# Kernel tuning notes

Measured on AMD Instinct MI355X. Metric: run time of the kernel, lower is better.

Reference implementation:

```python
import jax, jax.numpy as jnp
import numpy as np

NUM_CLASSES = 1000
EMB_DIM = 768
BATCH = 16384
EPS = 1e-8  # torch F.cosine_similarity eps


def setup_inputs() -> dict:
    key = jax.random.key(0)
    k1, k2, k3, k4 = jax.random.split(key, 4)
    embeddings = jax.random.normal(k1, (BATCH, EMB_DIM), dtype=jnp.float32)
    logits = jax.random.normal(k2, (BATCH, NUM_CLASSES), dtype=jnp.float32)
    targets = jax.random.randint(k3, (BATCH,), 0, NUM_CLASSES, dtype=jnp.int64 if jax.config.jax_enable_x64 else jnp.int32)
    centroids = jax.random.normal(k4, (NUM_CLASSES, EMB_DIM), dtype=jnp.float32)
    u = jnp.ones((1,), dtype=jnp.float32)
    return {"embeddings": embeddings, "logits": logits, "targets": targets,
            "centroids": centroids, "u": u}


def _cosine_sim(embeddings, centroids):
    # torch cosine_similarity: x / max(||x||, eps); formulated as normalize + GEMM
    en = embeddings / jnp.maximum(jnp.linalg.norm(embeddings, axis=1, keepdims=True), EPS)
    cn = centroids / jnp.maximum(jnp.linalg.norm(centroids, axis=1, keepdims=True), EPS)
    return jnp.einsum('nd,cd->nc', en, cn)  # [N, C]


def reference(embeddings, logits, targets, centroids, u):
    n_classes = centroids.shape[0]
    # cross entropy (mean reduction)
    logp = jax.nn.log_softmax(logits, axis=1)
    ce_loss = -jnp.mean(jnp.take_along_axis(logp, targets[:, None], axis=1))

    sim = _cosine_sim(embeddings, centroids)            # [N, C]
    soft_labels = jax.nn.softmax(sim, axis=1)           # [N, C]

    hard_one_hot = jax.nn.one_hot(targets, n_classes, dtype=jnp.float32)
    similarity_to_target = jnp.sum(soft_labels * hard_one_hot, axis=1)  # [N]
    discount = 1.0 - similarity_to_target
    reg_term = jnp.mean(discount) * u                   # shape (1,)

    # mse_loss(hard_one_hot, soft_labels.detach()) -- soft_labels detached
    dist_reg = jnp.mean((hard_one_hot - jax.lax.stop_gradient(soft_labels)) ** 2)

    return ce_loss + dist_reg + reg_term                # shape (1,)
```

## Files before the change

kernel.cpp:

```cpp
#include <hip/hip_runtime.h>
#include <hip/hip_bf16.h>
#include <stdint.h>

#define BATCH 16384
#define NCLS 1000
#define NPAD 1024
#define EMB 768
#define KT 12
#define BM 128
#define BN 256
#define ABYTES 8192
#define BUFB 24576
#define GEMM_BLKS 512
#define PREP_MAIN 2048
#define PREP_CENT 128

typedef __attribute__((ext_vector_type(4))) float f32x4;
typedef long v2i64 __attribute__((ext_vector_type(2)));

#define GLOAD16(g, l) __builtin_amdgcn_global_load_lds(              \
    (const __attribute__((address_space(1))) unsigned int*)(g),       \
    (__attribute__((address_space(3))) unsigned int*)(l), 16, 0, 0)

__device__ __forceinline__ float d4(float4 v) {
    return v.x*v.x + v.y*v.y + v.z*v.z + v.w*v.w;
}
__device__ __forceinline__ float e4(float4 v) {
    return __expf(v.x) + __expf(v.y) + __expf(v.z) + __expf(v.w);
}
__device__ __forceinline__ unsigned int pk8(float4 v, float s) {
    int p = 0;
    p = __builtin_amdgcn_cvt_pk_fp8_f32(v.x * s, v.y * s, p, false);
    p = __builtin_amdgcn_cvt_pk_fp8_f32(v.z * s, v.w * s, p, true);
    return (unsigned int)p;
}

__global__ __launch_bounds__(256, 4) void prep_ce(
    const float* __restrict__ emb, const float* __restrict__ cent,
    const float* __restrict__ logits, const int* __restrict__ targets,
    unsigned int* __restrict__ en8, unsigned int* __restrict__ cn8,
    float* __restrict__ ce_row)
{
    const int b    = blockIdx.x;
    const int lane = threadIdx.x & 63;
    const int w    = threadIdx.x >> 6;

    if (b < PREP_MAIN) {
        const int e0 = b * 8 + w * 2;
        const float4* a0 = (const float4*)(emb + (size_t)e0 * EMB);
        const float4* a1 = (const float4*)(emb + (size_t)(e0 + 1) * EMB);
        const float4* r0 = (const float4*)(logits + (size_t)e0 * NCLS);
        const float4* r1 = (const float4*)(logits + (size_t)(e0 + 1) * NCLS);

        float4 ea0 = a0[lane], ea1 = a0[lane + 64], ea2 = a0[lane + 128];
        float4 eb0 = a1[lane], eb1 = a1[lane + 64], eb2 = a1[lane + 128];
        float4 la0 = r0[lane], la1 = r0[lane + 64], la2 = r0[lane + 128];
        float4 lb0 = r1[lane], lb1 = r1[lane + 64], lb2 = r1[lane + 128];
        const bool has = lane < 58;
        float4 la3 = has ? r0[lane + 192] : la0;
        float4 lb3 = has ? r1[lane + 192] : lb0;
        const int t0 = targets[e0], t1 = targets[e0 + 1];
        const float xt0 = logits[(size_t)e0 * NCLS + t0];
        const float xt1 = logits[(size_t)(e0 + 1) * NCLS + t1];

        float ss0 = d4(ea0) + d4(ea1) + d4(ea2);
        float ss1 = d4(eb0) + d4(eb1) + d4(eb2);
        #pragma unroll
        for (int m = 1; m < 64; m <<= 1) {
            ss0 += __shfl_xor(ss0, m, 64);
            ss1 += __shfl_xor(ss1, m, 64);
        }
        const float sc0 = 1.0f / fmaxf(sqrtf(ss0), 1e-8f);
        const float sc1 = 1.0f / fmaxf(sqrtf(ss1), 1e-8f);
        unsigned int* o0 = en8 + (size_t)e0 * (EMB / 4);
        unsigned int* o1 = o0 + (EMB / 4);
        o0[lane] = pk8(ea0, sc0); o0[lane + 64] = pk8(ea1, sc0); o0[lane + 128] = pk8(ea2, sc0);
        o1[lane] = pk8(eb0, sc1); o1[lane + 64] = pk8(eb1, sc1); o1[lane + 128] = pk8(eb2, sc1);

        float s0 = e4(la0) + e4(la1) + e4(la2);
        float s1 = e4(lb0) + e4(lb1) + e4(lb2);
        if (has) { s0 += e4(la3); s1 += e4(lb3); }
        #pragma unroll
        for (int m = 1; m < 64; m <<= 1) {
            s0 += __shfl_xor(s0, m, 64);
            s1 += __shfl_xor(s1, m, 64);
        }
        if (lane == 0) {
            ce_row[e0]     = __logf(s0) - xt0;
            ce_row[e0 + 1] = __logf(s1) - xt1;
        }
        return;
    }

    const int c0 = (b - PREP_MAIN) * 8 + w * 2;
    #pragma unroll
    for (int p = 0; p < 2; ++p) {
        const int row = c0 + p;
        float4 v0 = {0,0,0,0}, v1 = {0,0,0,0}, v2 = {0,0,0,0};
        if (row < NCLS) {
            const float4* rp = (const float4*)(cent + (size_t)row * EMB);
            v0 = rp[lane]; v1 = rp[lane + 64]; v2 = rp[lane + 128];
        }
        float ss = d4(v0) + d4(v1) + d4(v2);
        #pragma unroll
        for (int m = 1; m < 64; m <<= 1) ss += __shfl_xor(ss, m, 64);
        const float sc = (row < NCLS) ? (1.0f / fmaxf(sqrtf(ss), 1e-8f)) : 0.0f;
        unsigned int* op = cn8 + (size_t)row * (EMB / 4);
        op[lane] = pk8(v0, sc); op[lane + 64] = pk8(v1, sc); op[lane + 128] = pk8(v2, sc);
    }
}

__global__ __launch_bounds__(256, 2) void gemm_kernel(
    const uint8_t* __restrict__ en8, const uint8_t* __restrict__ cn8,
    const int* __restrict__ targets,
    float* __restrict__ partZ, float* __restrict__ partS2,
    float* __restrict__ et_out)
{
    __shared__ __align__(128) uint8_t lds[2][BUFB];

    const int bid  = blockIdx.x;
    const int tid  = threadIdx.x;
    const int lane = tid & 63;
    const int warp = tid >> 6;

    const int g   = bid & 7;
    const int s   = bid >> 3;
    const int mb  = g * 16 + (s >> 2);
    const int nb  = s & 3;
    const int R0  = mb * BM;
    const int Nc0 = nb * BN;
    const int wr  = warp >> 1;
    const int wc  = warp & 1;
    const int l15 = lane & 15;
    const int rq  = lane >> 4;

    const int csw  = ((tid & 3) * 16) ^ (((tid >> 3) & 3) << 4);
    const int srow = tid >> 2;
    size_t asrc[2], bsrc[4];
    #pragma unroll
    for (int j = 0; j < 2; ++j) asrc[j] = (size_t)(R0  + j * 64 + srow) * EMB + csw;
    #pragma unroll
    for (int j = 0; j < 4; ++j) bsrc[j] = (size_t)(Nc0 + j * 64 + srow) * EMB + csw;
    const uint8_t* enb = en8;
    const uint8_t* cnb = cn8;

#define STAGE(b, kt) do { const size_t ko = (size_t)(kt) * 64;               \
    _Pragma("unroll") for (int j = 0; j < 2; ++j)                            \
        GLOAD16(enb + asrc[j] + ko, &lds[b][j * 4096 + tid * 16]);           \
    _Pragma("unroll") for (int j = 0; j < 4; ++j)                            \
        GLOAD16(cnb + bsrc[j] + ko, &lds[b][ABYTES + j * 4096 + tid * 16]);  \
} while (0)

    const int cx   = (rq * 16) ^ (((l15 >> 1) & 3) << 4);
    const int aoff = (wr * 64 + l15) * 64 + cx;
    const int boff = ABYTES + (wc * 128 + l15) * 64 + cx;

    f32x4 acc[4][8];
    #pragma unroll
    for (int m = 0; m < 4; ++m)
        #pragma unroll
        for (int n = 0; n < 8; ++n) acc[m][n] = (f32x4){0.f, 0.f, 0.f, 0.f};

    STAGE(0, 0);
    __syncthreads();

    for (int kt = 0; kt < KT; ++kt) {
        const int buf = kt & 1;
        if (kt + 1 < KT) STAGE(buf ^ 1, kt + 1);
        const uint8_t* L = &lds[buf][0];
        v2i64 af[4], bf[8];
        #pragma unroll
        for (int m = 0; m < 4; ++m) af[m] = *(const v2i64*)(L + aoff + m * 1024);
        #pragma unroll
        for (int n = 0; n < 8; ++n) bf[n] = *(const v2i64*)(L + boff + n * 1024);
        #pragma unroll
        for (int kk = 0; kk < 2; ++kk)
            #pragma unroll
            for (int m = 0; m < 4; ++m)
                #pragma unroll
                for (int n = 0; n < 8; ++n)
                    acc[m][n] = __builtin_amdgcn_mfma_f32_16x16x32_fp8_fp8(
                        bf[n][kk], af[m][kk], acc[m][n], 0, 0, 0);
        __syncthreads();
    }
#undef STAGE

    const int plane = nb * 2 + wc;
    #pragma unroll
    for (int m = 0; m < 4; ++m) {
        const int row = R0 + wr * 64 + m * 16 + l15;
        const int t   = targets[row];
        float z = 0.f, s2 = 0.f;
        #pragma unroll
        for (int n = 0; n < 8; ++n) {
            const int cb = Nc0 + wc * 128 + n * 16 + rq * 4;
            #pragma unroll
            for (int r = 0; r < 4; ++r) {
                const bool valid = (cb + r) < NCLS;
                float e = valid ? __expf(acc[m][n][r]) : 0.f;
                z += e; s2 += e * e;
                if (cb + r == t) et_out[row] = e;
            }
        }
        z  += __shfl_xor(z, 16, 64);  z  += __shfl_xor(z, 32, 64);
        s2 += __shfl_xor(s2, 16, 64); s2 += __shfl_xor(s2, 32, 64);
        if (rq == 0) {
            partZ [(size_t)plane * BATCH + row] = z;
            partS2[(size_t)plane * BATCH + row] = s2;
        }
    }
}

__global__ __launch_bounds__(256) void finalize_kernel(
    const float* __restrict__ partZ, const float* __restrict__ partS2,
    const float* __restrict__ et_out, const float* __restrict__ ce_row,
    const float* __restrict__ u, float* __restrict__ out)
{
    __shared__ float red[4];
    const int row  = blockIdx.x * 256 + threadIdx.x;
    const int lane = threadIdx.x & 63;
    float z = 0.f, s2 = 0.f;
    #pragma unroll
    for (int i = 0; i < 8; ++i) {
        z  += partZ [(size_t)i * BATCH + row];
        s2 += partS2[(size_t)i * BATCH + row];
    }
    float et = et_out[row];
    float invz = 1.0f / z;
    float pt = et * invz;
    float c = (s2 * invz * invz - 2.0f * pt + 1.0f) * (1.0f / ((float)BATCH * (float)NCLS))
            + (1.0f - pt) * u[0] * (1.0f / (float)BATCH)
            + ce_row[row] * (1.0f / (float)BATCH);
    #pragma unroll
    for (int m = 1; m < 64; m <<= 1) c += __shfl_xor(c, m, 64);
    if (lane == 0) red[threadIdx.x >> 6] = c;
    __syncthreads();
    if (threadIdx.x == 0) atomicAdd(out, red[0] + red[1] + red[2] + red[3]);
}

extern "C" void kernel_launch(void* const* d_in, const int* in_sizes, int n_in,
                              void* d_out, int out_size, void* d_ws, size_t ws_size,
                              hipStream_t stream) {
    const float* emb       = (const float*)d_in[0];
    const float* logits    = (const float*)d_in[1];
    const int*   targets   = (const int*)d_in[2];
    const float* centroids = (const float*)d_in[3];
    const float* u         = (const float*)d_in[4];
    float* out = (float*)d_out;

    uint8_t* en8  = (uint8_t*)d_ws;
    uint8_t* cn8  = en8 + (size_t)BATCH * EMB;
    float* partZ  = (float*)(cn8 + (size_t)NPAD * EMB);
    float* partS2 = partZ + 8 * BATCH;
    float* et_out = partS2 + 8 * BATCH;
    float* ce_row = et_out + BATCH;

    hipMemsetAsync(d_out, 0, sizeof(float), stream);
    prep_ce<<<PREP_MAIN + PREP_CENT, 256, 0, stream>>>(emb, centroids, logits, targets,
                                                       (unsigned int*)en8, (unsigned int*)cn8, ce_row);
    gemm_kernel<<<GEMM_BLKS, 256, 0, stream>>>(en8, cn8, targets, partZ, partS2, et_out);
    finalize_kernel<<<BATCH / 256, 256, 0, stream>>>(partZ, partS2, et_out, ce_row, u, out);
}
```

Before: 55.03 us.

## Use one block per row in prep and replace atomic memset with two-stage reduction

The prep kernel now assigns one 256-thread block to each embedding/logit row and each centroid row, with 16384+1024 blocks instead of 2176. Each thread loads a single float4, and the reduction runs through LDS with a __syncthreads. The finalize step writes per-block partials that a second tiny kernel sums, which drops the hipMemsetAsync and the atomicAdd. Each thread now has less work and less latency per thread, but the change brings many more small blocks, a block-level barrier and an extra kernel launch.

Result: faster. 50.68 us (-7.9%).

```diff
diff --git a/kernel.cpp b/kernel.cpp
--- a/kernel.cpp
+++ b/kernel.cpp
@@ -12,8 +12,6 @@
 #define ABYTES 8192
 #define BUFB 24576
 #define GEMM_BLKS 512
-#define PREP_MAIN 2048
-#define PREP_CENT 128
 
 typedef __attribute__((ext_vector_type(4))) float f32x4;
 typedef long v2i64 __attribute__((ext_vector_type(2)));
@@ -35,79 +33,61 @@
     return (unsigned int)p;
 }
 
-__global__ __launch_bounds__(256, 4) void prep_ce(
+__global__ __launch_bounds__(256) void prep_row(
     const float* __restrict__ emb, const float* __restrict__ cent,
     const float* __restrict__ logits, const int* __restrict__ targets,
     unsigned int* __restrict__ en8, unsigned int* __restrict__ cn8,
     float* __restrict__ ce_row)
 {
+    __shared__ float ssp[4], esp[4], xts;
     const int b    = blockIdx.x;
-    const int lane = threadIdx.x & 63;
-    const int w    = threadIdx.x >> 6;
-
-    if (b < PREP_MAIN) {
-        const int e0 = b * 8 + w * 2;
-        const float4* a0 = (const float4*)(emb + (size_t)e0 * EMB);
-        const float4* a1 = (const float4*)(emb + (size_t)(e0 + 1) * EMB);
-        const float4* r0 = (const float4*)(logits + (size_t)e0 * NCLS);
-        const float4* r1 = (const float4*)(logits + (size_t)(e0 + 1) * NCLS);
-
-        float4 ea0 = a0[lane], ea1 = a0[lane + 64], ea2 = a0[lane + 128];
-        float4 eb0 = a1[lane], eb1 = a1[lane + 64], eb2 = a1[lane + 128];
-        float4 la0 = r0[lane], la1 = r0[lane + 64], la2 = r0[lane + 128];
-        float4 lb0 = r1[lane], lb1 = r1[lane + 64], lb2 = r1[lane + 128];
-        const bool has = lane < 58;
-        float4 la3 = has ? r0[lane + 192] : la0;
-        float4 lb3 = has ? r1[lane + 192] : lb0;
-        const int t0 = targets[e0], t1 = targets[e0 + 1];
-        const float xt0 = logits[(size_t)e0 * NCLS + t0];
-        const float xt1 = logits[(size_t)(e0 + 1) * NCLS + t1];
-
-        float ss0 = d4(ea0) + d4(ea1) + d4(ea2);
-        float ss1 = d4(eb0) + d4(eb1) + d4(eb2);
+    const int tid  = threadIdx.x;
+    const int w    = tid >> 6;
+    const int lane = tid & 63;
+
+    if (b < BATCH) {
+        const float4* er = (const float4*)(emb + (size_t)b * EMB);
+        const float4* lr = (const float4*)(logits + (size_t)b * NCLS);
+        const bool he = tid < 192;
+        const bool hl = tid < 250;
+        float4 ev = he ? er[tid] : make_float4(0.f, 0.f, 0.f, 0.f);
+        float4 lv = hl ? lr[tid] : make_float4(0.f, 0.f, 0.f, 0.f);
+        if (tid == 254) {
+            const int t = targets[b];
+            xts = logits[(size_t)b * NCLS + t];
+        }
+        float ss = d4(ev);
+        float es = hl ? e4(lv) : 0.f;
         #pragma unroll
         for (int m = 1; m < 64; m <<= 1) {
-            ss0 += __shfl_xor(ss0, m, 64);
-            ss1 += __shfl_xor(ss1, m, 64);
-        }
-        const float sc0 = 1.0f / fmaxf(sqrtf(ss0), 1e-8f);
-        const float sc1 = 1.0f / fmaxf(sqrtf(ss1), 1e-8f);
-        unsigned int* o0 = en8 + (size_t)e0 * (EMB / 4);
-        unsigned int* o1 = o0 + (EMB / 4);
-        o0[lane] = pk8(ea0, sc0); o0[lane + 64] = pk8(ea1, sc0); o0[lane + 128] = pk8(ea2, sc0);
-        o1[lane] = pk8(eb0, sc1); o1[lane + 64] = pk8(eb1, sc1); o1[lane + 128] = pk8(eb2, sc1);
-
-        float s0 = e4(la0) + e4(la1) + e4(la2);
-        float s1 = e4(lb0) + e4(lb1) + e4(lb2);
-        if (has) { s0 += e4(la3); s1 += e4(lb3); }
-        #pragma unroll
-        for (int m = 1; m < 64; m <<= 1) {
-            s0 += __shfl_xor(s0, m, 64);
-            s1 += __shfl_xor(s1, m, 64);
-        }
-        if (lane == 0) {
-            ce_row[e0]     = __logf(s0) - xt0;
-            ce_row[e0 + 1] = __logf(s1) - xt1;
+            ss += __shfl_xor(ss, m, 64);
+            es += __shfl_xor(es, m, 64);
+        }
+        if (lane == 0) { ssp[w] = ss; esp[w] = es; }
+        __syncthreads();
+        const float sstot = ssp[0] + ssp[1] + ssp[2] + ssp[3];
+        const float sc = 1.0f / fmaxf(sqrtf(sstot), 1e-8f);
+        if (he) en8[(size_t)b * (EMB / 4) + tid] = pk8(ev, sc);
+        if (tid == 0) {
+            const float estot = esp[0] + esp[1] + esp[2] + esp[3];
+            ce_row[b] = __logf(estot) - xts;
         }
         return;
     }
 
-    const int c0 = (b - PREP_MAIN) * 8 + w * 2;
-    #pragma unroll
-    for (int p = 0; p < 2; ++p) {
-        const int row = c0 + p;
-        float4 v0 = {0,0,0,0}, v1 = {0,0,0,0}, v2 = {0,0,0,0};
-        if (row < NCLS) {
-            const float4* rp = (const float4*)(cent + (size_t)row * EMB);
-            v0 = rp[lane]; v1 = rp[lane + 64]; v2 = rp[lane + 128];
-        }
-        float ss = d4(v0) + d4(v1) + d4(v2);
-        #pragma unroll
-        for (int m = 1; m < 64; m <<= 1) ss += __shfl_xor(ss, m, 64);
-        const float sc = (row < NCLS) ? (1.0f / fmaxf(sqrtf(ss), 1e-8f)) : 0.0f;
-        unsigned int* op = cn8 + (size_t)row * (EMB / 4);
-        op[lane] = pk8(v0, sc); op[lane + 64] = pk8(v1, sc); op[lane + 128] = pk8(v2, sc);
-    }
+    const int row = b - BATCH;
+    const bool hv = row < NCLS;
+    const bool he = tid < 192 && hv;
+    const float4* cr = (const float4*)(cent + (size_t)row * EMB);
+    float4 cv = he ? cr[tid] : make_float4(0.f, 0.f, 0.f, 0.f);
+    float ss = d4(cv);
+    #pragma unroll
+    for (int m = 1; m < 64; m <<= 1) ss += __shfl_xor(ss, m, 64);
+    if (lane == 0) ssp[w] = ss;
+    __syncthreads();
+    const float sstot = ssp[0] + ssp[1] + ssp[2] + ssp[3];
+    const float sc = hv ? (1.0f / fmaxf(sqrtf(sstot), 1e-8f)) : 0.0f;
+    if (tid < 192) cn8[(size_t)row * (EMB / 4) + tid] = he ? pk8(cv, sc) : 0u;
 }
 
 __global__ __launch_bounds__(256, 2) void gemm_kernel(
@@ -211,10 +191,10 @@
     }
 }
 
-__global__ __launch_bounds__(256) void finalize_kernel(
+__global__ __launch_bounds__(256) void finalize1(
     const float* __restrict__ partZ, const float* __restrict__ partS2,
     const float* __restrict__ et_out, const float* __restrict__ ce_row,
-    const float* __restrict__ u, float* __restrict__ out)
+    const float* __restrict__ u, float* __restrict__ fpart)
 {
     __shared__ float red[4];
     const int row  = blockIdx.x * 256 + threadIdx.x;
@@ -235,7 +215,17 @@
     for (int m = 1; m < 64; m <<= 1) c += __shfl_xor(c, m, 64);
     if (lane == 0) red[threadIdx.x >> 6] = c;
     __syncthreads();
-    if (threadIdx.x == 0) atomicAdd(out, red[0] + red[1] + red[2] + red[3]);
+    if (threadIdx.x == 0) fpart[blockIdx.x] = red[0] + red[1] + red[2] + red[3];
+}
+
+__global__ __launch_bounds__(64) void finalize2(
+    const float* __restrict__ fpart, float* __restrict__ out)
+{
+    const int lane = threadIdx.x;
+    float s = fpart[lane];
+    #pragma unroll
+    for (int m = 1; m < 64; m <<= 1) s += __shfl_xor(s, m, 64);
+    if (lane == 0) out[0] = s;
 }
 
 extern "C" void kernel_launch(void* const* d_in, const int* in_sizes, int n_in,
@@ -254,10 +244,11 @@
     float* partS2 = partZ + 8 * BATCH;
     float* et_out = partS2 + 8 * BATCH;
     float* ce_row = et_out + BATCH;
-
-    hipMemsetAsync(d_out, 0, sizeof(float), stream);
-    prep_ce<<<PREP_MAIN + PREP_CENT, 256, 0, stream>>>(emb, centroids, logits, targets,
-                                                       (unsigned int*)en8, (unsigned int*)cn8, ce_row);
+    float* fpart  = ce_row + BATCH;
+
+    prep_row<<<BATCH + NPAD, 256, 0, stream>>>(emb, centroids, logits, targets,
+                                               (unsigned int*)en8, (unsigned int*)cn8, ce_row);
     gemm_kernel<<<GEMM_BLKS, 256, 0, stream>>>(en8, cn8, targets, partZ, partS2, et_out);
-    finalize_kernel<<<BATCH / 256, 256, 0, stream>>>(partZ, partS2, et_out, ce_row, u, out);
-}
+    finalize1<<<BATCH / 256, 256, 0, stream>>>(partZ, partS2, et_out, ce_row, u, fpart);
+    finalize2<<<1, 64, 0, stream>>>(fpart, out);
+}
```
